# Optimization experiments

Measured on AMD Instinct MI355X. Metric: run time of the kernel, lower is better.

The kernel has to match this reference:

```python
import jax, jax.numpy as jnp
import numpy as np

DIM = 128
HEADS = 8
HD = DIM // HEADS          # 16
KS = 8                     # neighborhood kernel size
STRIDE = 2                 # GNA query-group stride
DIL = 2                    # dilation


def axis_indices(L, k, s, d):
    """Per-axis neighborhood indices [L, k] for dilated, strided, edge-clamped NA.

    Queries are grouped in blocks of `s`; every query in a block shares the
    window of the block's center query (GNA 'stride'). Dilation partitions the
    axis into `d` sub-grids; the window lives on the center query's sub-grid
    and is clamped so it never leaves the axis (natten-style sliding window).
    """
    idx = np.zeros((L, k), dtype=np.int32)
    for i in range(L):
        ic = min((i // s) * s + (s - 1) // 2, L - 1)   # group-center query
        r = ic % d                                      # sub-grid (residue)
        Lsub = (L - r + d - 1) // d                     # sub-grid length
        ii = ic // d                                    # index within sub-grid
        start = min(max(ii - (k - 1) // 2, 0), max(Lsub - k, 0))
        for j in range(k):
            idx[i, j] = r + d * min(start + j, Lsub - 1)
    return idx


def setup_inputs() -> dict:
    key = jax.random.key(0)
    ks = jax.random.split(key, 5)
    x = jax.random.normal(ks[0], (1, DIM, 96, 96), jnp.float32)
    # depthwise-grouped qkv conv: Conv2d(dim, 3*dim, 3, 1, 1, groups=dim)
    qkv_w = jax.random.normal(ks[1], (3 * DIM, 1, 3, 3), jnp.float32) * 0.1
    qkv_b = jax.random.normal(ks[2], (3 * DIM,), jnp.float32) * 0.02
    # 1x1 projection: Conv2d(dim, dim, 1)
    proj_w = jax.random.normal(ks[3], (DIM, DIM, 1, 1), jnp.float32) * (DIM ** -0.5)
    proj_b = jax.random.normal(ks[4], (DIM,), jnp.float32) * 0.02
    return {"x": x, "qkv_w": qkv_w, "qkv_b": qkv_b, "proj_w": proj_w, "proj_b": proj_b}


def reference(x, qkv_w, qkv_b, proj_w, proj_b):
    B, C, H, W = x.shape
    # grouped (groups=C) 3x3 conv producing q,k,v
    qkv = jax.lax.conv_general_dilated(
        x, qkv_w, window_strides=(1, 1), padding=[(1, 1), (1, 1)],
        dimension_numbers=("NCHW", "OIHW", "NCHW"), feature_group_count=C)
    qkv = qkv + qkv_b[None, :, None, None]
    qkv = qkv.reshape(B, 3, C, H, W)

    def to_heads(t):  # b c h w -> b h w nh hd
        return t.reshape(B, HEADS, HD, H, W).transpose(0, 3, 4, 1, 2)

    q = to_heads(qkv[:, 0])
    k = to_heads(qkv[:, 1])
    v = to_heads(qkv[:, 2])

    scale = HD ** -0.5
    ri = jnp.asarray(axis_indices(H, KS, STRIDE, DIL))  # [H, KS]
    ci = jnp.asarray(axis_indices(W, KS, STRIDE, DIL))  # [W, KS]
    R = ri[:, :, None, None]       # [H, KS, 1, 1]
    Cc = ci[None, None, :, :]      # [1, 1, W, KS]
    k_win = k[:, R, Cc]            # [B, H, KS, W, KS, nh, hd]
    v_win = v[:, R, Cc]

    logits = jnp.einsum("bijnd,bipjqnd->bijnpq", q * scale, k_win)
    attn = jax.nn.softmax(logits.reshape(B, H, W, HEADS, KS * KS), axis=-1)
    attn = attn.reshape(B, H, W, HEADS, KS, KS)
    out = jnp.einsum("bijnpq,bipjqnd->bijnd", attn, v_win)

    out = out.transpose(0, 3, 4, 1, 2).reshape(B, C, H, W)  # b h w nh hd -> b c h w
    out = jnp.einsum("bchw,oc->bohw", out, proj_w[:, :, 0, 0]) + proj_b[None, :, None, None]
    return out
```

## Files before the change

kernel.cpp:

```cpp
#include <hip/hip_runtime.h>
#include <hip/hip_bf16.h>

#define HH   96
#define WW   96
#define NPIX 9216
#define CH   128
#define NH   8
#define HD   16
#define KS   8

#define NEPIX   2304
#define NPOS    120
#define KVPITCH 40
#define QTPITCH 136
#define KVTPITCH 264

__device__ __forceinline__ unsigned short f2bf(float f) {
    __hip_bfloat16 b = __float2bfloat16(f);
    union { __hip_bfloat16 b; unsigned short u; } cv; cv.b = b; return cv.u;
}
__device__ __forceinline__ void u4_to_f8(uint4 u, float* f) {
    f[0] = __uint_as_float(u.x << 16); f[1] = __uint_as_float(u.x & 0xffff0000u);
    f[2] = __uint_as_float(u.y << 16); f[3] = __uint_as_float(u.y & 0xffff0000u);
    f[4] = __uint_as_float(u.z << 16); f[5] = __uint_as_float(u.z & 0xffff0000u);
    f[6] = __uint_as_float(u.w << 16); f[7] = __uint_as_float(u.w & 0xffff0000u);
}

__global__ __launch_bounds__(256) void conv_kernel(
    const float* __restrict__ x,
    const float* __restrict__ w,
    const float* __restrict__ bias,
    unsigned short* __restrict__ q_pm,
    unsigned short* __restrict__ kv_pm)
{
    __shared__ unsigned short qt [24 * QTPITCH];
    __shared__ unsigned short kvt[12 * KVTPITCH];

    const int row = blockIdx.x >> 2;
    const int qtr = blockIdx.x & 3;
    const int j0q = qtr * 24;
    const int tid = threadIdx.x;
    const int g   = tid >> 1;
    const int sh  = tid & 1;
    const int j0  = j0q + sh * 12;
    const bool kvrow = (row & 1) == 0;

    const float* xg = x + g * NPIX;

    float xr[3][14];
    #pragma unroll
    for (int dr = 0; dr < 3; ++dr) {
        const int r = row + dr - 1;
        if (r >= 0 && r < HH) {
            #pragma unroll
            for (int m = 0; m < 14; ++m) {
                const int j = j0 + m - 1;
                xr[dr][m] = (j >= 0 && j < WW) ? xg[r * WW + j] : 0.f;
            }
        } else {
            #pragma unroll
            for (int m = 0; m < 14; ++m) xr[dr][m] = 0.f;
        }
    }

    #pragma unroll
    for (int dt = 0; dt < 3; ++dt) {
        const int o = 3 * g + dt;
        const int t = o >> 7;
        const int c = o & 127;
        float w9[9];
        #pragma unroll
        for (int k = 0; k < 9; ++k) w9[k] = w[o * 9 + k];
        const float b = bias[o];

        if (t == 0) {
            #pragma unroll
            for (int px = 0; px < 12; ++px) {
                float acc = b;
                #pragma unroll
                for (int kh = 0; kh < 3; ++kh)
                    #pragma unroll
                    for (int kw = 0; kw < 3; ++kw)
                        acc += xr[kh][px + kw] * w9[kh * 3 + kw];
                qt[(sh * 12 + px) * QTPITCH + c] = f2bf(acc);
            }
        } else if (kvrow) {
            #pragma unroll
            for (int pe = 0; pe < 6; ++pe) {
                const int px = pe * 2;
                float acc = b;
                #pragma unroll
                for (int kh = 0; kh < 3; ++kh)
                    #pragma unroll
                    for (int kw = 0; kw < 3; ++kw)
                        acc += xr[kh][px + kw] * w9[kh * 3 + kw];
                kvt[(sh * 6 + pe) * KVTPITCH + (t - 1) * CH + c] = f2bf(acc);
            }
        }
    }

    __syncthreads();

    const int ntask = kvrow ? 768 : 384;
    #pragma unroll
    for (int it = 0; it < 3; ++it) {
        const int idx = it * 256 + tid;
        if (idx < 384) {
            const int px  = idx >> 4;
            const int c8  = (idx & 15) * 8;
            const uint4 v = *(const uint4*)&qt[px * QTPITCH + c8];
            *(uint4*)(q_pm + ((size_t)(row * WW) + j0q + px) * CH + c8) = v;
        } else if (idx < ntask) {
            const int k2  = idx - 384;
            const int epx = k2 >> 5;
            const int c32 = (k2 & 31) * 8;
            const int t1  = c32 >> 7;
            const int c   = c32 & 127;
            const uint4 v = *(const uint4*)&kvt[epx * KVTPITCH + c32];
            *(uint4*)(kv_pm + ((size_t)t1 * NEPIX + (row >> 1) * 48
                               + (j0q >> 1) + epx) * CH + c) = v;
        }
    }
}

__global__ __launch_bounds__(256) void attn_kernel(
    const unsigned short* __restrict__ q_pm,
    const unsigned short* __restrict__ kv_pm,
    float* __restrict__ a_t)
{
    __shared__ unsigned short kv[2][NPOS * KVPITCH];

    const int tid = threadIdx.x;
    const int seg = blockIdx.x;
    const int hp  = blockIdx.y;
    const int i   = seg / 6;
    const int j0  = (seg - i * 6) * 16;
    const int rs     = 2 * min(max(i / 2 - 3, 0), 40);
    const int cs_min = 2 * min(max(j0 / 2 - 3, 0), 40);
    const int er0 = rs >> 1;
    const int ec0 = cs_min >> 1;

    #pragma unroll
    for (int it = 0; it < 4; ++it) {
        const int idx = it * 256 + tid;
        if (idx < 960) {
            const int kvsel = idx / 480;
            const int rem   = idx - kvsel * 480;
            const int pos   = rem >> 2;
            const int sub   = rem & 3;
            const int p     = pos / 15;
            const int cc    = pos - p * 15;
            const int ec    = min(ec0 + cc, 47);
            const int ep    = (er0 + p) * 48 + ec;
            *(uint4*)&kv[kvsel][pos * KVPITCH + sub * 8] =
                *(const uint4*)(kv_pm + ((size_t)kvsel * NEPIX + ep) * CH
                                + hp * 32 + sub * 8);
        }
    }

    const int lane  = tid & 63;
    const int wave  = tid >> 6;
    const int r     = lane >> 3;
    const int hh    = (lane >> 2) & 1;
    const int px    = wave * 4 + (lane & 3);
    const int h     = hp * 2 + hh;
    const int pix   = seg * 16 + px;
    const int j     = j0 + px;
    const int ci0   = (2 * min(max(j / 2 - 3, 0), 40) - cs_min) >> 1;

    float qr[HD];
    {
        const unsigned short* qp = q_pm + (size_t)pix * CH + h * HD;
        u4_to_f8(*(const uint4*)qp, qr);
        u4_to_f8(*(const uint4*)(qp + 8), qr + 8);
        #pragma unroll
        for (int d = 0; d < HD; ++d) qr[d] *= 0.25f;
    }

    __syncthreads();

    const int posr = r * 15 + ci0;
    float lg[KS];
    float m = -1e30f;
    #pragma unroll
    for (int q = 0; q < KS; ++q) {
        const unsigned short* kp = &kv[0][(posr + q) * KVPITCH + hh * HD];
        float kf[HD];
        u4_to_f8(*(const uint4*)kp, kf);
        u4_to_f8(*(const uint4*)(kp + 8), kf + 8);
        float acc = 0.f;
        #pragma unroll
        for (int d = 0; d < HD; ++d) acc += qr[d] * kf[d];
        lg[q] = acc;
        m = fmaxf(m, acc);
    }

    float s = 0.f;
    #pragma unroll
    for (int q = 0; q < KS; ++q) { lg[q] = __expf(lg[q] - m); s += lg[q]; }

    float o[HD];
    #pragma unroll
    for (int d = 0; d < HD; ++d) o[d] = 0.f;
    #pragma unroll
    for (int q = 0; q < KS; ++q) {
        const unsigned short* vp = &kv[1][(posr + q) * KVPITCH + hh * HD];
        float vf[HD];
        u4_to_f8(*(const uint4*)vp, vf);
        u4_to_f8(*(const uint4*)(vp + 8), vf + 8);
        const float wgt = lg[q];
        #pragma unroll
        for (int d = 0; d < HD; ++d) o[d] += wgt * vf[d];
    }

    #pragma unroll
    for (int mask = 8; mask <= 32; mask <<= 1) {
        const float m2 = __shfl_xor(m, mask);
        const float s2 = __shfl_xor(s, mask);
        const float mn = fmaxf(m, m2);
        const float ea = __expf(m - mn);
        const float eb = __expf(m2 - mn);
        s = s * ea + s2 * eb;
        #pragma unroll
        for (int d = 0; d < HD; ++d) {
            const float o2 = __shfl_xor(o[d], mask);
            o[d] = o[d] * ea + o2 * eb;
        }
        m = mn;
    }
    const float inv = 1.f / s;

    a_t[(size_t)(h * HD + 2 * r)     * NPIX + pix] = o[2 * r]     * inv;
    a_t[(size_t)(h * HD + 2 * r + 1) * NPIX + pix] = o[2 * r + 1] * inv;
}

__global__ __launch_bounds__(256) void proj_kernel(
    const float* __restrict__ a_t,
    const float* __restrict__ pw,
    const float* __restrict__ pb,
    float* __restrict__ out)
{
    const int idx = blockIdx.x * 256 + threadIdx.x;
    const int op  = __builtin_amdgcn_readfirstlane(idx / 2304);
    const int pq  = idx - op * 2304;
    const int px0 = pq * 4;
    const int o0  = op * 2;

    float acc0[4], acc1[4];
    #pragma unroll
    for (int e = 0; e < 4; ++e) { acc0[e] = pb[o0]; acc1[e] = pb[o0 + 1]; }

    for (int c = 0; c < CH; ++c) {
        const float4 a  = *(const float4*)(a_t + (size_t)c * NPIX + px0);
        const float  w0 = pw[(o0)     * CH + c];
        const float  w1 = pw[(o0 + 1) * CH + c];
        acc0[0] += a.x * w0; acc0[1] += a.y * w0; acc0[2] += a.z * w0; acc0[3] += a.w * w0;
        acc1[0] += a.x * w1; acc1[1] += a.y * w1; acc1[2] += a.z * w1; acc1[3] += a.w * w1;
    }

    *(float4*)(out + (size_t)(o0)     * NPIX + px0) = make_float4(acc0[0], acc0[1], acc0[2], acc0[3]);
    *(float4*)(out + (size_t)(o0 + 1) * NPIX + px0) = make_float4(acc1[0], acc1[1], acc1[2], acc1[3]);
}

extern "C" void kernel_launch(void* const* d_in, const int* in_sizes, int n_in,
                              void* d_out, int out_size, void* d_ws, size_t ws_size,
                              hipStream_t stream)
{
    const float* x      = (const float*)d_in[0];
    const float* qkv_w  = (const float*)d_in[1];
    const float* qkv_b  = (const float*)d_in[2];
    const float* proj_w = (const float*)d_in[3];
    const float* proj_b = (const float*)d_in[4];
    float* out = (float*)d_out;

    unsigned short* q_pm  = (unsigned short*)d_ws;
    unsigned short* kv_pm = q_pm + (size_t)NPIX * CH;
    float*          a_t   = (float*)(kv_pm + (size_t)2 * NEPIX * CH);

    conv_kernel<<<384, 256, 0, stream>>>(x, qkv_w, qkv_b, q_pm, kv_pm);
    attn_kernel<<<dim3(576, 4), 256, 0, stream>>>(q_pm, kv_pm, a_t);
    proj_kernel<<<576, 256, 0, stream>>>(a_t, proj_w, proj_b, out);
}
```

Measured before the change: 103.6 us.

## Tile projection GEMM with shared-memory activation tile and 4x4 register blocking

The 1x1 projection kernel used to have each thread compute 2 output channels by 4 pixels, re-reading every activation column from global memory for each output-channel pair. Now each block stages a 128-channel by 32-pixel activation tile in LDS and each thread computes a 4x4 output block, loading weights as float4. This cuts global reads of the intermediate activations by reusing them across all 128 output channels within the block. The grid shrinks to 288 blocks, which may lower occupancy across the CUs.

```diff
diff --git a/kernel.cpp b/kernel.cpp
--- a/kernel.cpp
+++ b/kernel.cpp
@@ -240,26 +240,60 @@
     const float* __restrict__ pb,
     float* __restrict__ out)
 {
-    const int idx = blockIdx.x * 256 + threadIdx.x;
-    const int op  = __builtin_amdgcn_readfirstlane(idx / 2304);
-    const int pq  = idx - op * 2304;
-    const int px0 = pq * 4;
-    const int o0  = op * 2;
-
-    float acc0[4], acc1[4];
-    #pragma unroll
-    for (int e = 0; e < 4; ++e) { acc0[e] = pb[o0]; acc1[e] = pb[o0 + 1]; }
-
-    for (int c = 0; c < CH; ++c) {
-        const float4 a  = *(const float4*)(a_t + (size_t)c * NPIX + px0);
-        const float  w0 = pw[(o0)     * CH + c];
-        const float  w1 = pw[(o0 + 1) * CH + c];
-        acc0[0] += a.x * w0; acc0[1] += a.y * w0; acc0[2] += a.z * w0; acc0[3] += a.w * w0;
-        acc1[0] += a.x * w1; acc1[1] += a.y * w1; acc1[2] += a.z * w1; acc1[3] += a.w * w1;
-    }
-
-    *(float4*)(out + (size_t)(o0)     * NPIX + px0) = make_float4(acc0[0], acc0[1], acc0[2], acc0[3]);
-    *(float4*)(out + (size_t)(o0 + 1) * NPIX + px0) = make_float4(acc1[0], acc1[1], acc1[2], acc1[3]);
+    __shared__ float at[CH][36];
+
+    const int tid = threadIdx.x;
+    const int px0 = blockIdx.x * 32;
+
+    #pragma unroll
+    for (int it = 0; it < 4; ++it) {
+        const int idx = it * 256 + tid;
+        const int c   = idx >> 3;
+        const int p4  = (idx & 7) * 4;
+        *(float4*)&at[c][p4] =
+            *(const float4*)(a_t + (size_t)c * NPIX + px0 + p4);
+    }
+    __syncthreads();
+
+    const int og = tid >> 3;
+    const int o0 = og * 4;
+    const int p0 = (tid & 7) * 4;
+
+    float acc[4][4];
+    #pragma unroll
+    for (int i = 0; i < 4; ++i) {
+        const float b = pb[o0 + i];
+        #pragma unroll
+        for (int j = 0; j < 4; ++j) acc[i][j] = b;
+    }
+
+    #pragma unroll 2
+    for (int c0 = 0; c0 < CH; c0 += 4) {
+        float4 wv[4];
+        #pragma unroll
+        for (int i = 0; i < 4; ++i)
+            wv[i] = *(const float4*)(pw + (size_t)(o0 + i) * CH + c0);
+        float4 av[4];
+        #pragma unroll
+        for (int k = 0; k < 4; ++k)
+            av[k] = *(const float4*)&at[c0 + k][p0];
+        #pragma unroll
+        for (int i = 0; i < 4; ++i) {
+            acc[i][0] += wv[i].x * av[0].x; acc[i][1] += wv[i].x * av[0].y;
+            acc[i][2] += wv[i].x * av[0].z; acc[i][3] += wv[i].x * av[0].w;
+            acc[i][0] += wv[i].y * av[1].x; acc[i][1] += wv[i].y * av[1].y;
+            acc[i][2] += wv[i].y * av[1].z; acc[i][3] += wv[i].y * av[1].w;
+            acc[i][0] += wv[i].z * av[2].x; acc[i][1] += wv[i].z * av[2].y;
+            acc[i][2] += wv[i].z * av[2].z; acc[i][3] += wv[i].z * av[2].w;
+            acc[i][0] += wv[i].w * av[3].x; acc[i][1] += wv[i].w * av[3].y;
+            acc[i][2] += wv[i].w * av[3].z; acc[i][3] += wv[i].w * av[3].w;
+        }
+    }
+
+    #pragma unroll
+    for (int i = 0; i < 4; ++i)
+        *(float4*)(out + (size_t)(o0 + i) * NPIX + px0 + p0)
+            = make_float4(acc[i][0], acc[i][1], acc[i][2], acc[i][3]);
 }
 
 extern "C" void kernel_launch(void* const* d_in, const int* in_sizes, int n_in,
@@ -279,5 +313,5 @@
 
     conv_kernel<<<384, 256, 0, stream>>>(x, qkv_w, qkv_b, q_pm, kv_pm);
     attn_kernel<<<dim3(576, 4), 256, 0, stream>>>(q_pm, kv_pm, a_t);
-    proj_kernel<<<576, 256, 0, stream>>>(a_t, proj_w, proj_b, out);
-}
+    proj_kernel<<<288, 256, 0, stream>>>(a_t, proj_w, proj_b, out);
+}
```

Result: faster. 99.70 us (-3.8%).
